# Performance work log

Hardware: AMD Instinct MI355X
Metric: run time of the kernel (lower is better)

Reference implementation:

```python
import jax, jax.numpy as jnp
import numpy as np

B, L, H, V, HALF = 128, 4096, 64, 64, 32
ALPHA = 0.95
LN_EPS = 1e-5


def _normalize(x):
    # torch F.normalize(dim=-1): x / max(||x||_2, 1e-12)
    n = jnp.linalg.norm(x, axis=-1, keepdims=True)
    return x / jnp.maximum(n, 1e-12)


def setup_inputs() -> dict:
    key = jax.random.key(0)
    ks = jax.random.split(key, 17)
    s = 0.05
    return {
        "seq": jax.random.randint(ks[0], (B, L), 0, V),
        "embed": jax.random.normal(ks[1], (V, H), jnp.float32),
        "W1": jax.random.normal(ks[2], (H, 2 * H), jnp.float32) * s,
        "b1": jnp.zeros((2 * H,), jnp.float32),
        "W2": jax.random.normal(ks[3], (2 * H, H), jnp.float32) * s,
        "b2": jnp.zeros((H,), jnp.float32),
        "gamma": jnp.ones((H,), jnp.float32),
        "beta": jnp.zeros((H,), jnp.float32),
        "Ws": jax.random.normal(ks[4], (H, HALF), jnp.float32) * s,
        "bs": jnp.zeros((HALF,), jnp.float32),
        "We": jax.random.normal(ks[5], (H, HALF), jnp.float32) * s,
        "be": jnp.zeros((HALF,), jnp.float32),
        "Wrp": jax.random.normal(ks[6], (2 * HALF, H), jnp.float32) * s,
        "brp": jnp.zeros((H,), jnp.float32),
        "Wout": jax.random.normal(ks[7], (H, V), jnp.float32) * s,
        "bout": jnp.zeros((V,), jnp.float32),
    }


def _forward(seq, embed, W1, b1, W2, b2, gamma, beta,
             Ws, bs, We, be, Wrp, brp, Wout, bout):
    # Encoder: embed + FF(ReLU) residual + LayerNorm
    h0 = embed[seq]                                   # [B,L,H]
    ff = jnp.maximum(h0 @ W1 + b1, 0.0) @ W2 + b2
    x = h0 + ff
    mu = x.mean(-1, keepdims=True)
    var = ((x - mu) ** 2).mean(-1, keepdims=True)
    h = (x - mu) / jnp.sqrt(var + LN_EPS) * gamma + beta  # [B,L,H]

    # Precompute per-step projections for t = 0 .. L-2
    hp = h[:, :-1, :]                                 # [B,L-1,H]
    hs = hp @ Ws + bs                                 # [B,L-1,HALF]
    he = hp @ We + be
    ksn = _normalize(hs)
    ken = _normalize(he)
    scale = (jnp.arange(L - 1, dtype=h.dtype) + 1.0) / L  # (t+1)/L

    def step(carry, inp):
        M_s, M_e = carry                              # [B,HALF,HALF]
        hs_t, he_t, ks_t, ke_t, sc = inp
        vps = jnp.einsum('bij,bj->bi', M_s, ks_t)
        vpe = jnp.einsum('bij,bj->bi', M_e, ke_t)
        M_s = M_s + (1.0 - ALPHA) * (hs_t - vps)[:, :, None] * ks_t[:, None, :]
        M_e = M_e + (1.0 - ALPHA) * sc * (he_t - vpe)[:, :, None] * ke_t[:, None, :]
        return (M_s, M_e), None

    xs = (jnp.swapaxes(hs, 0, 1), jnp.swapaxes(he, 0, 1),
          jnp.swapaxes(ksn, 0, 1), jnp.swapaxes(ken, 0, 1), scale)
    M0 = jnp.zeros((B, HALF, HALF), h.dtype)
    (M_s, M_e), _ = jax.lax.scan(step, (M0, M0), xs)

    # Read with last-token query
    q = h[:, -1, :]
    qs = _normalize(q @ Ws + bs)
    qe = _normalize(q @ We + be)
    rs = jnp.einsum('bij,bj->bi', M_s, qs)
    re = jnp.einsum('bij,bj->bi', M_e, qe)
    r = jnp.concatenate([rs, re], axis=-1)            # [B,2*HALF]
    return (r @ Wrp + brp) @ Wout + bout              # [B,V]


def reference(seq, embed, W1, b1, W2, b2, gamma, beta,
              Ws, bs, We, be, Wrp, brp, Wout, bout):
    return _forward(seq, embed, W1, b1, W2, b2, gamma, beta,
                    Ws, bs, We, be, Wrp, brp, Wout, bout)
```

## Files before the change

### kernel.cpp

```cpp
#include <hip/hip_runtime.h>
#include <hip/hip_bf16.h>
#include <stdint.h>


#define BETA 0.05f
#define NB 128
#define NL 4096
#define TC 16
#define NCH 256
#define NBLD 6
#define SLOT_F 1360
#define NSLOT 12

#define L_GR   (NSLOT * SLOT_F)
#define L_DA   (L_GR + 4096)
#define L_RV   (L_DA + 64)
#define L_O1   (L_RV + 64)
#define L_WHO  (L_O1 + 64)
#define L_TOT  (L_WHO + 1)

struct Ptrs { const void* p[15]; };

__device__ inline float readlane_f(float v, int l) {
    return __int_as_float(__builtin_amdgcn_readlane(__float_as_int(v), l));
}
__device__ inline float bperm_f(int idx, float v) {
    return __int_as_float(__builtin_amdgcn_ds_bpermute(idx, __float_as_int(v)));
}
__device__ inline float ldT(const float* p, int i) { return p[i]; }
__device__ inline float ldT(const __hip_bfloat16* p, int i) { return __bfloat162float(p[i]); }

template <typename T>
__device__ void build_tables_body(const T* emb, const T* W1, const T* b1,
                                  const T* W2, const T* b2, const T* gam,
                                  const T* bet, const T* Wsm, const T* bsv,
                                  const T* Wem, const T* bev, float* tbl)
{
    int v = blockIdx.x;
    int j = threadIdx.x;
    __shared__ float h0s[64];
    __shared__ float act[128];
    __shared__ float hrow[64];

    float h0 = ldT(emb, v * 64 + j);
    h0s[j] = h0;
    __syncthreads();

    float za = ldT(b1, j);
    float zb = ldT(b1, j + 64);
    for (int k = 0; k < 64; ++k) {
        float hk = h0s[k];
        za = fmaf(hk, ldT(W1, k * 128 + j), za);
        zb = fmaf(hk, ldT(W1, k * 128 + j + 64), zb);
    }
    act[j] = fmaxf(za, 0.0f);
    act[j + 64] = fmaxf(zb, 0.0f);
    __syncthreads();

    float ff = ldT(b2, j);
    for (int k = 0; k < 128; ++k)
        ff = fmaf(act[k], ldT(W2, k * 64 + j), ff);
    float x = h0 + ff;

    float s = x;
    for (int off = 32; off >= 1; off >>= 1) s += __shfl_xor(s, off, 64);
    float mu = s * (1.0f / 64.0f);
    float d = x - mu;
    float s2 = d * d;
    for (int off = 32; off >= 1; off >>= 1) s2 += __shfl_xor(s2, off, 64);
    float var = s2 * (1.0f / 64.0f);
    float h = d / sqrtf(var + 1e-5f) * ldT(gam, j) + ldT(bet, j);
    hrow[j] = h;
    __syncthreads();

    if (j < 32) {
        float sv = ldT(bsv, j);
        for (int k = 0; k < 64; ++k)
            sv = fmaf(hrow[k], ldT(Wsm, k * 32 + j), sv);
        float n2 = sv * sv;
        for (int off = 16; off >= 1; off >>= 1) n2 += __shfl_xor(n2, off, 64);
        float nrm = fmaxf(sqrtf(n2), 1e-12f);
        tbl[v * 32 + j] = sv;
        tbl[2048 + v * 32 + j] = sv / nrm;
    } else {
        int jj = j - 32;
        float ev = ldT(bev, jj);
        for (int k = 0; k < 64; ++k)
            ev = fmaf(hrow[k], ldT(Wem, k * 32 + jj), ev);
        float n2 = ev * ev;
        for (int off = 16; off >= 1; off >>= 1) n2 += __shfl_xor(n2, off, 64);
        float nrm = fmaxf(sqrtf(n2), 1e-12f);
        tbl[4096 + v * 32 + jj] = ev;
        tbl[6144 + v * 32 + jj] = ev / nrm;
    }
}

__global__ __launch_bounds__(64, 2) void build_tables(Ptrs ps, float* __restrict__ tbl,
                                                      int* __restrict__ flags)
{
    if (blockIdx.x == 0) {
        flags[threadIdx.x] = 0;
        flags[threadIdx.x + 64] = 0;
    }
    uint32_t g0 = *(const uint32_t*)ps.p[5];
    if (g0 == 0x3F803F80u)
        build_tables_body((const __hip_bfloat16*)ps.p[0], (const __hip_bfloat16*)ps.p[1],
                          (const __hip_bfloat16*)ps.p[2], (const __hip_bfloat16*)ps.p[3],
                          (const __hip_bfloat16*)ps.p[4], (const __hip_bfloat16*)ps.p[5],
                          (const __hip_bfloat16*)ps.p[6], (const __hip_bfloat16*)ps.p[7],
                          (const __hip_bfloat16*)ps.p[8], (const __hip_bfloat16*)ps.p[9],
                          (const __hip_bfloat16*)ps.p[10], tbl);
    else
        build_tables_body((const float*)ps.p[0], (const float*)ps.p[1],
                          (const float*)ps.p[2], (const float*)ps.p[3],
                          (const float*)ps.p[4], (const float*)ps.p[5],
                          (const float*)ps.p[6], (const float*)ps.p[7],
                          (const float*)ps.p[8], (const float*)ps.p[9],
                          (const float*)ps.p[10], tbl);
}

__global__ __launch_bounds__(512, 2) void ema_ms(
    const int* __restrict__ seq, const float* __restrict__ tbl,
    Ptrs ps, float* __restrict__ rvbuf, int* __restrict__ flags,
    void* __restrict__ outv)
{
    __shared__ float S[L_TOT];

    int bm = blockIdx.x;
    int b = bm >> 1, mat = bm & 1;
    int tid = threadIdx.x;
    int wid = tid >> 6, lane = tid & 63;
    const float bstep = BETA / 4096.0f;

    if (tid < 64) S[L_DA + tid] = 0.0f;

    const float* ktab = tbl + 2048 + mat * 4096;
    for (int i = tid; i < 2048; i += 512)
        S[(i >> 5) * 33 + (i & 31)] = ktab[i];
    __syncthreads();

    {
        float Kown[32];
#pragma unroll
        for (int j = 0; j < 32; ++j) Kown[j] = S[lane * 33 + j];
        for (int v8 = 0; v8 < 8; ++v8) {
            int vt = wid * 8 + v8;
            float acc = 0.0f;
#pragma unroll
            for (int j = 0; j < 32; ++j)
                acc = fmaf(S[vt * 33 + j], Kown[j], acc);
            S[L_GR + vt * 64 + lane] = acc;
        }
    }
    __syncthreads();

    const int* sb = seq + (size_t)b * NL;
    float y = 0.0f;
    if (wid == 0) {
        int vlast = sb[NL - 1];
        y = S[L_GR + vlast * 64 + lane];
    }

    const int NRND = (NCH + NBLD - 1) / NBLD;

    for (int r = 0; r <= NRND; ++r) {
        if (wid != 0 && wid != 4) {
            int bi = (wid > 4) ? (wid - 2) : (wid - 1);
            int ci = NBLD * r + bi;
            if (r < NRND && ci < NCH) {
                int c = NCH - 1 - ci;
                float* slot = S + ((r & 1) * NBLD + bi) * SLOT_F;
                int tokv = 0; float bneg = 0.0f;
                if (lane < TC) {
                    int t = c * TC + (TC - 1) - lane;
                    tokv = sb[t];
                    float bb = mat ? bstep * (float)(t + 1) : BETA;
                    if (t == NL - 1) bb = 0.0f;
                    bneg = -bb;
                    ((int*)(slot + 1344))[lane] = tokv;
                }
                float garr[TC];
#pragma unroll
                for (int p = 0; p < TC; ++p) {
                    int vp = __builtin_amdgcn_readlane(tokv, p);
                    const float* gr = S + L_GR + vp * 64;
                    slot[320 + p * 64 + lane] = gr[lane];
                    garr[p] = gr[tokv] * bneg;
                }
                float x[TC];
                x[0] = (lane == 0) ? 1.0f : 0.0f;
#pragma unroll
                for (int p = 1; p < TC; ++p) {
                    float xp = (lane == p) ? 1.0f : 0.0f;
#pragma unroll
                    for (int j = 0; j < p; ++j)
                        xp = fmaf(readlane_f(garr[p], j), x[j], xp);
                    x[p] = xp;
                }
                if (lane < TC) {
#pragma unroll
                    for (int p = 0; p < TC; ++p)
                        slot[p * 20 + lane] = x[p];
                }
            }
        } else if (wid == 0 && r >= 1) {
            for (int bi = 0; bi < NBLD; ++bi) {
                int ci = NBLD * (r - 1) + bi;
                if (ci >= NCH) break;
                int c = NCH - 1 - ci;
                float* slot = S + (((r - 1) & 1) * NBLD + bi) * SLOT_F;
                int tokf = (lane < TC) ? ((int*)(slot + 1344))[lane] : 0;
                float bv = 0.0f;
                if (lane < TC) {
                    int t = c * TC + (TC - 1) - lane;
                    float bb = mat ? bstep * (float)(t + 1) : BETA;
                    if (t == NL - 1) bb = 0.0f;
                    bv = bb;
                }
                float ry = bperm_f(tokf << 2, y);
                const float4* vr = (const float4*)(slot + (lane & 15) * 20);
                float4 v0 = vr[0], v1 = vr[1], v2 = vr[2], v3 = vr[3];
                float s0 = v0.x * readlane_f(ry, 0);
                float s1 = v0.y * readlane_f(ry, 1);
                float s2 = v0.z * readlane_f(ry, 2);
                float s3 = v0.w * readlane_f(ry, 3);
                s0 = fmaf(v1.x, readlane_f(ry, 4), s0);
                s1 = fmaf(v1.y, readlane_f(ry, 5), s1);
                s2 = fmaf(v1.z, readlane_f(ry, 6), s2);
                s3 = fmaf(v1.w, readlane_f(ry, 7), s3);
                s0 = fmaf(v2.x, readlane_f(ry, 8), s0);
                s1 = fmaf(v2.y, readlane_f(ry, 9), s1);
                s2 = fmaf(v2.z, readlane_f(ry, 10), s2);
                s3 = fmaf(v2.w, readlane_f(ry, 11), s3);
                s0 = fmaf(v3.x, readlane_f(ry, 12), s0);
                s1 = fmaf(v3.y, readlane_f(ry, 13), s1);
                s2 = fmaf(v3.z, readlane_f(ry, 14), s2);
                s3 = fmaf(v3.w, readlane_f(ry, 15), s3);
                float dv = ((s0 + s1) + (s2 + s3)) * bv;
                if (lane < TC) atomicAdd(&S[L_DA + tokf], dv);
                float dn = -dv;
                float ya = 0.f, yb = 0.f, yc = 0.f, yd = 0.f;
#pragma unroll
                for (int p = 0; p < TC; p += 4) {
                    ya = fmaf(readlane_f(dn, p),     slot[320 + (p)     * 64 + lane], ya);
                    yb = fmaf(readlane_f(dn, p + 1), slot[320 + (p + 1) * 64 + lane], yb);
                    yc = fmaf(readlane_f(dn, p + 2), slot[320 + (p + 2) * 64 + lane], yc);
                    yd = fmaf(readlane_f(dn, p + 3), slot[320 + (p + 3) * 64 + lane], yd);
                }
                y += (ya + yb) + (yc + yd);
            }
        }
        __syncthreads();
    }

    if (tid < 32) {
        float rr = 0.0f;
        const float* hsrc = tbl + mat * 4096;
        for (int v = 0; v < 64; ++v)
            rr = fmaf(S[L_DA + v], hsrc[v * 32 + tid], rr);
        __hip_atomic_store(&rvbuf[bm * 32 + tid], rr,
                           __ATOMIC_RELAXED, __HIP_MEMORY_SCOPE_AGENT);
    }
    __syncthreads();
    if (tid == 0) {
        int old = __hip_atomic_fetch_add(&flags[b], 1,
                                         __ATOMIC_ACQ_REL, __HIP_MEMORY_SCOPE_AGENT);
        ((int*)S)[L_WHO] = old;
    }
    __syncthreads();
    if (((int*)S)[L_WHO] != 1) return;

    if (tid < 64)
        S[L_RV + tid] = __hip_atomic_load(&rvbuf[b * 64 + tid],
                                          __ATOMIC_RELAXED, __HIP_MEMORY_SCOPE_AGENT);
    __syncthreads();

    uint32_t g0h = *(const uint32_t*)ps.p[5];
    int isbf = (g0h == 0x3F803F80u) ? 1 : 0;
    if (tid < 64) {
        float o;
        if (isbf) {
            const __hip_bfloat16* W = (const __hip_bfloat16*)ps.p[11];
            o = __bfloat162float(((const __hip_bfloat16*)ps.p[12])[tid]);
            for (int i = 0; i < 64; ++i)
                o = fmaf(S[L_RV + i], __bfloat162float(W[i * 64 + tid]), o);
        } else {
            const float* W = (const float*)ps.p[11];
            o = ((const float*)ps.p[12])[tid];
            for (int i = 0; i < 64; ++i)
                o = fmaf(S[L_RV + i], W[i * 64 + tid], o);
        }
        S[L_O1 + tid] = o;
    }
    __syncthreads();
    if (tid < 64) {
        float o2;
        if (isbf) {
            const __hip_bfloat16* W = (const __hip_bfloat16*)ps.p[13];
            o2 = __bfloat162float(((const __hip_bfloat16*)ps.p[14])[tid]);
            for (int i = 0; i < 64; ++i)
                o2 = fmaf(S[L_O1 + i], __bfloat162float(W[i * 64 + tid]), o2);
            ((__hip_bfloat16*)outv)[b * 64 + tid] = __float2bfloat16(o2);
        } else {
            const float* W = (const float*)ps.p[13];
            o2 = ((const float*)ps.p[14])[tid];
            for (int i = 0; i < 64; ++i)
                o2 = fmaf(S[L_O1 + i], W[i * 64 + tid], o2);
            ((float*)outv)[b * 64 + tid] = o2;
        }
    }
}

extern "C" void kernel_launch(void* const* d_in, const int* in_sizes, int n_in,
                              void* d_out, int out_size, void* d_ws, size_t ws_size,
                              hipStream_t stream) {
    const int* seq = (const int*)d_in[0];
    Ptrs ps;
    for (int i = 0; i < 15; ++i) ps.p[i] = d_in[i + 1];

    float* tbl = (float*)d_ws;
    float* rvbuf = tbl + 8192;
    int* flags = (int*)(rvbuf + 8192);

    build_tables<<<64, 64, 0, stream>>>(ps, tbl, flags);
    ema_ms<<<NB * 2, 512, 0, stream>>>(seq, tbl, ps, rvbuf, flags, d_out);
}
```

Before: 200.0 us.

## Prefetch next chunk's Gram rows in sequential wave and shrink LDS slots

Builder waves no longer copy 16 Gram-table rows per chunk into LDS slots. The sequential wave 0 now reads those rows directly from the shared Gram table and software-pipelines them: it loads the next chunk's tokens, triangular solve vectors and Gram rows into registers while computing the current chunk. The goal is to take LDS load latency off the serial critical path and to cut builder-side LDS traffic. Slot size shrinks accordingly. Launch bounds drop to one block per SM, which raises the register budget for the prefetch buffers but may reduce occupancy.

```diff
diff --git a/kernel.cpp b/kernel.cpp
--- a/kernel.cpp
+++ b/kernel.cpp
@@ -9,7 +9,7 @@
 #define TC 16
 #define NCH 256
 #define NBLD 6
-#define SLOT_F 1360
+#define SLOT_F 336
 #define NSLOT 12
 
 #define L_GR   (NSLOT * SLOT_F)
@@ -119,7 +119,7 @@
                           (const float*)ps.p[10], tbl);
 }
 
-__global__ __launch_bounds__(512, 2) void ema_ms(
+__global__ __launch_bounds__(512, 1) void ema_ms(
     const int* __restrict__ seq, const float* __restrict__ tbl,
     Ptrs ps, float* __restrict__ rvbuf, int* __restrict__ flags,
     void* __restrict__ outv)
@@ -177,15 +177,13 @@
                     float bb = mat ? bstep * (float)(t + 1) : BETA;
                     if (t == NL - 1) bb = 0.0f;
                     bneg = -bb;
-                    ((int*)(slot + 1344))[lane] = tokv;
+                    ((int*)(slot + 320))[lane] = tokv;
                 }
                 float garr[TC];
 #pragma unroll
                 for (int p = 0; p < TC; ++p) {
                     int vp = __builtin_amdgcn_readlane(tokv, p);
-                    const float* gr = S + L_GR + vp * 64;
-                    slot[320 + p * 64 + lane] = gr[lane];
-                    garr[p] = gr[tokv] * bneg;
+                    garr[p] = S[L_GR + vp * 64 + tokv] * bneg;
                 }
                 float x[TC];
                 x[0] = (lane == 0) ? 1.0f : 0.0f;
@@ -204,12 +202,44 @@
                 }
             }
         } else if (wid == 0 && r >= 1) {
-            for (int bi = 0; bi < NBLD; ++bi) {
-                int ci = NBLD * (r - 1) + bi;
-                if (ci >= NCH) break;
+            int rpar = ((r - 1) & 1) * NBLD;
+            int base_ci = NBLD * (r - 1);
+            int nch_r = NCH - base_ci;
+            if (nch_r > NBLD) nch_r = NBLD;
+
+            float* slot0 = S + rpar * SLOT_F;
+            int tokc = ((int*)(slot0 + 320))[lane & 15];
+            const float4* vr0 = (const float4*)(slot0 + (lane & 15) * 20);
+            float4 Vc0 = vr0[0], Vc1 = vr0[1], Vc2 = vr0[2], Vc3 = vr0[3];
+            float gpc[16];
+#pragma unroll
+            for (int p = 0; p < 16; ++p) {
+                int vp = __builtin_amdgcn_readlane(tokc, p);
+                gpc[p] = S[L_GR + vp * 64 + lane];
+            }
+
+            for (int bi = 0; bi < nch_r; ++bi) {
+                int ci = base_ci + bi;
                 int c = NCH - 1 - ci;
-                float* slot = S + (((r - 1) & 1) * NBLD + bi) * SLOT_F;
-                int tokf = (lane < TC) ? ((int*)(slot + 1344))[lane] : 0;
+                float ry = bperm_f(tokc << 2, y);
+
+                int tokn = 0;
+                float4 Vn0, Vn1, Vn2, Vn3;
+                float gpn[16];
+                bool hasn = (bi + 1 < nch_r);
+                if (hasn) {
+                    float* slotn = S + (rpar + bi + 1) * SLOT_F;
+                    tokn = ((int*)(slotn + 320))[lane & 15];
+                    const float4* vr = (const float4*)(slotn + (lane & 15) * 20);
+                    Vn0 = vr[0]; Vn1 = vr[1]; Vn2 = vr[2]; Vn3 = vr[3];
+#pragma unroll
+                    for (int p = 0; p < 16; ++p) {
+                        int vp = __builtin_amdgcn_readlane(tokn, p);
+                        gpn[p] = S[L_GR + vp * 64 + lane];
+                    }
+                }
+                asm volatile("" ::: "memory");
+
                 float bv = 0.0f;
                 if (lane < TC) {
                     int t = c * TC + (TC - 1) - lane;
@@ -217,37 +247,41 @@
                     if (t == NL - 1) bb = 0.0f;
                     bv = bb;
                 }
-                float ry = bperm_f(tokf << 2, y);
-                const float4* vr = (const float4*)(slot + (lane & 15) * 20);
-                float4 v0 = vr[0], v1 = vr[1], v2 = vr[2], v3 = vr[3];
-                float s0 = v0.x * readlane_f(ry, 0);
-                float s1 = v0.y * readlane_f(ry, 1);
-                float s2 = v0.z * readlane_f(ry, 2);
-                float s3 = v0.w * readlane_f(ry, 3);
-                s0 = fmaf(v1.x, readlane_f(ry, 4), s0);
-                s1 = fmaf(v1.y, readlane_f(ry, 5), s1);
-                s2 = fmaf(v1.z, readlane_f(ry, 6), s2);
-                s3 = fmaf(v1.w, readlane_f(ry, 7), s3);
-                s0 = fmaf(v2.x, readlane_f(ry, 8), s0);
-                s1 = fmaf(v2.y, readlane_f(ry, 9), s1);
-                s2 = fmaf(v2.z, readlane_f(ry, 10), s2);
-                s3 = fmaf(v2.w, readlane_f(ry, 11), s3);
-                s0 = fmaf(v3.x, readlane_f(ry, 12), s0);
-                s1 = fmaf(v3.y, readlane_f(ry, 13), s1);
-                s2 = fmaf(v3.z, readlane_f(ry, 14), s2);
-                s3 = fmaf(v3.w, readlane_f(ry, 15), s3);
+                float s0 = Vc0.x * readlane_f(ry, 0);
+                float s1 = Vc0.y * readlane_f(ry, 1);
+                float s2 = Vc0.z * readlane_f(ry, 2);
+                float s3 = Vc0.w * readlane_f(ry, 3);
+                s0 = fmaf(Vc1.x, readlane_f(ry, 4), s0);
+                s1 = fmaf(Vc1.y, readlane_f(ry, 5), s1);
+                s2 = fmaf(Vc1.z, readlane_f(ry, 6), s2);
+                s3 = fmaf(Vc1.w, readlane_f(ry, 7), s3);
+                s0 = fmaf(Vc2.x, readlane_f(ry, 8), s0);
+                s1 = fmaf(Vc2.y, readlane_f(ry, 9), s1);
+                s2 = fmaf(Vc2.z, readlane_f(ry, 10), s2);
+                s3 = fmaf(Vc2.w, readlane_f(ry, 11), s3);
+                s0 = fmaf(Vc3.x, readlane_f(ry, 12), s0);
+                s1 = fmaf(Vc3.y, readlane_f(ry, 13), s1);
+                s2 = fmaf(Vc3.z, readlane_f(ry, 14), s2);
+                s3 = fmaf(Vc3.w, readlane_f(ry, 15), s3);
                 float dv = ((s0 + s1) + (s2 + s3)) * bv;
-                if (lane < TC) atomicAdd(&S[L_DA + tokf], dv);
+                if (lane < TC) atomicAdd(&S[L_DA + tokc], dv);
                 float dn = -dv;
-                float ya = 0.f, yb = 0.f, yc = 0.f, yd = 0.f;
+                float ya = 0.f, yb = 0.f, yc2 = 0.f, yd = 0.f;
 #pragma unroll
                 for (int p = 0; p < TC; p += 4) {
-                    ya = fmaf(readlane_f(dn, p),     slot[320 + (p)     * 64 + lane], ya);
-                    yb = fmaf(readlane_f(dn, p + 1), slot[320 + (p + 1) * 64 + lane], yb);
-                    yc = fmaf(readlane_f(dn, p + 2), slot[320 + (p + 2) * 64 + lane], yc);
-                    yd = fmaf(readlane_f(dn, p + 3), slot[320 + (p + 3) * 64 + lane], yd);
-                }
-                y += (ya + yb) + (yc + yd);
+                    ya  = fmaf(readlane_f(dn, p),     gpc[p],     ya);
+                    yb  = fmaf(readlane_f(dn, p + 1), gpc[p + 1], yb);
+                    yc2 = fmaf(readlane_f(dn, p + 2), gpc[p + 2], yc2);
+                    yd  = fmaf(readlane_f(dn, p + 3), gpc[p + 3], yd);
+                }
+                y += (ya + yb) + (yc2 + yd);
+
+                if (hasn) {
+                    tokc = tokn;
+                    Vc0 = Vn0; Vc1 = Vn1; Vc2 = Vn2; Vc3 = Vn3;
+#pragma unroll
+                    for (int p = 0; p < 16; ++p) gpc[p] = gpn[p];
+                }
             }
         }
         __syncthreads();
```

After: 215.0 us. 7.5% more time.
